# Kernel optimization log

Hardware: AMD Instinct MI355X
Metric: run time of the kernel (lower is better)

Reference implementation:

```python
import jax, jax.numpy as jnp
import numpy as np

K_MASK = -2.3819763e+38
NUM_HEADS = 16
NUM_KV_HEADS = 8
HEAD_DIM = 128
FEATURES = 2048
QUERY_SCALE = 0.08838834764831845  # head_dim ** -0.5
ROPE_BASE = 10000
SOFT_CAP = 50.0
WINDOW = 1024


def apply_rope(inputs, positions, base_frequency=ROPE_BASE):
    # inputs: [B, L, N, H], positions: [B, L]
    head_dim = inputs.shape[-1]
    fraction = 2.0 * jnp.arange(0, head_dim // 2, dtype=jnp.float32) / head_dim
    timescale = jnp.asarray(base_frequency, jnp.float32) ** fraction
    sinusoid = positions[..., None].astype(jnp.float32) / timescale[None, None, :]
    sinusoid = sinusoid[..., None, :]  # [B, L, 1, H/2]
    sin, cos = jnp.sin(sinusoid), jnp.cos(sinusoid)
    first, second = jnp.split(inputs, 2, axis=-1)
    out = jnp.concatenate([first * cos - second * sin,
                           second * cos + first * sin], axis=-1)
    return out.astype(inputs.dtype)


def setup_inputs() -> dict:
    key = jax.random.key(0)
    ks = jax.random.split(key, 4)
    B, T, D = 2, 2048, FEATURES
    x = jax.random.normal(ks[0], (B, T, D), dtype=jnp.float32)
    segment_pos = jnp.broadcast_to(jnp.arange(T, dtype=jnp.int32)[None, :], (B, T))
    # causal prefill mask [B, T, S] with S == T
    attn_mask = jnp.broadcast_to(
        jnp.tril(jnp.ones((T, T), dtype=bool))[None], (B, T, T))
    wq = jax.random.normal(ks[1], (NUM_HEADS, D, HEAD_DIM), dtype=jnp.float32) * 0.02
    wkv = jax.random.normal(ks[2], (2, NUM_KV_HEADS, D, HEAD_DIM), dtype=jnp.float32) * 0.02
    wo = jax.random.normal(ks[3], (NUM_HEADS, HEAD_DIM, D), dtype=jnp.float32) * 0.02
    return {"x": x, "segment_pos": segment_pos, "attn_mask": attn_mask,
            "wq": wq, "wkv": wkv, "wo": wo}


def reference(x, segment_pos, attn_mask, wq, wkv, wo):
    # Projections
    q = jnp.einsum('BTD,NDH->BTNH', x, wq)              # [B,T,N,H]
    kv = jnp.einsum('BSD,CKDH->CBSKH', x, wkv)          # [2,B,S,K,H]
    k, v = kv[0], kv[1]

    # RoPE + query scaling
    q = apply_rope(q, segment_pos) * QUERY_SCALE
    k = apply_rope(k, segment_pos)

    # GQA: fold query heads into (K groups, G heads per group)
    B, T, N, H = q.shape
    K, G = NUM_KV_HEADS, N // NUM_KV_HEADS
    qg = q.reshape(B, T, K, G, H)
    logits = jnp.einsum('BTKGH,BSKH->BTKGS', qg, k).reshape(B, T, N, -1)

    # Logit soft-capping
    logits = jnp.tanh(logits / SOFT_CAP) * SOFT_CAP

    # Sliding-window mask (prefill: end_index=0, cache_len = S)
    S = attn_mask.shape[-1]
    cache_positions = jnp.arange(S)[None, None, :]       # [1,1,S]
    sp = segment_pos[:, :, None]                         # [B,T,1]
    sliding = (cache_positions > sp - WINDOW) & (cache_positions < sp + WINDOW)
    mask = jnp.logical_and(attn_mask, sliding)

    padded = jnp.where(mask[:, :, None, :], logits, K_MASK)
    probs = jax.nn.softmax(padded, axis=-1).astype(k.dtype)

    pg = probs.reshape(B, T, K, G, S)
    encoded = jnp.einsum('BTKGS,BSKH->BTKGH', pg, v).reshape(B, T, N, H)
    return jnp.einsum('BTNH,NHD->BTD', encoded, wo)
```

## Files before the change

kernel.cpp:

```cpp
#include <hip/hip_runtime.h>

typedef __attribute__((ext_vector_type(8))) short short8;
typedef __attribute__((ext_vector_type(4))) float f32x4;
typedef __attribute__((ext_vector_type(4))) float f4;
typedef __attribute__((ext_vector_type(4))) unsigned short u16x4;

__device__ __forceinline__ unsigned short f2bf(float f) {
    union { float f; unsigned int u; } v; v.f = f;
    unsigned int r = v.u + 0x7fffu + ((v.u >> 16) & 1u);
    return (unsigned short)(r >> 16);
}
__device__ __forceinline__ float bf2f(unsigned short h) {
    union { unsigned int u; float f; } v; v.u = ((unsigned int)h) << 16;
    return v.f;
}
__device__ __forceinline__ void gload_lds16(const void* g, void* l) {
    __builtin_amdgcn_global_load_lds(
        (const __attribute__((address_space(1))) unsigned int*)g,
        (__attribute__((address_space(3))) unsigned int*)l, 16, 0, 0);
}


__global__ void conv_x(const float* __restrict__ x, unsigned short* __restrict__ xb) {
    int i = blockIdx.x * 256 + threadIdx.x;
    f4 v = ((const f4*)x)[i];
    u16x4 o;
    o[0] = f2bf(v[0]); o[1] = f2bf(v[1]); o[2] = f2bf(v[2]); o[3] = f2bf(v[3]);
    ((u16x4*)xb)[i] = o;
}

__global__ void conv_wqkvt(const float* __restrict__ wq, const float* __restrict__ wkv,
                           unsigned short* __restrict__ wt) {
    __shared__ float tile[64 * 65];
    const int d0 = blockIdx.x * 64, f0 = blockIdx.y * 64;
    const int head = f0 >> 7;
    const int h0 = f0 & 127;
    const float* src;
    if (head < 16) src = wq + (size_t)head * 2048 * 128;
    else           src = wkv + (size_t)(head - 16) * 2048 * 128;
    {
        int hh = threadIdx.x & 63, dq = threadIdx.x >> 6;
        #pragma unroll
        for (int r = 0; r < 16; ++r) {
            int dd = r * 4 + dq;
            tile[dd * 65 + hh] = src[(size_t)(d0 + dd) * 128 + h0 + hh];
        }
    }
    __syncthreads();
    {
        int dd = threadIdx.x & 63, fq = threadIdx.x >> 6;
        #pragma unroll
        for (int r = 0; r < 16; ++r) {
            int fl = r * 4 + fq;
            wt[(size_t)(f0 + fl) * 2048 + d0 + dd] = f2bf(tile[dd * 65 + fl]);
        }
    }
}

__global__ void conv_wot(const float* __restrict__ wo, unsigned short* __restrict__ wt) {
    __shared__ float tile[64 * 65];
    const int d0 = blockIdx.x * 64, r0 = blockIdx.y * 64;
    int cc = threadIdx.x & 63, rq = threadIdx.x >> 6;
    #pragma unroll
    for (int r = 0; r < 16; ++r) {
        int rr = r * 4 + rq;
        tile[rr * 65 + cc] = wo[(size_t)(r0 + rr) * 2048 + d0 + cc];
    }
    __syncthreads();
    #pragma unroll
    for (int r = 0; r < 16; ++r) {
        int rr = r * 4 + rq;
        wt[(size_t)(d0 + rr) * 2048 + r0 + cc] = f2bf(tile[cc * 65 + rr]);
    }
}


__global__ __launch_bounds__(512, 2)
void gemm8p(const unsigned short* __restrict__ A,
            const unsigned short* __restrict__ Bt,
            unsigned short* __restrict__ C, int M, int N, int K) {
    __shared__ __align__(16) unsigned short LDS[65536];
    const int tid = threadIdx.x, lane = tid & 63, w = tid >> 6;
    const int wr = w >> 2, wc = w & 3;
    const int l15 = lane & 15, l4 = lane >> 4;
    int nwg = gridDim.x * gridDim.y;
    int wg = blockIdx.y * gridDim.x + blockIdx.x;
    int swz = (wg & 7) * (nwg >> 3) + (wg >> 3);
    int bx = swz % gridDim.x, by = swz / gridDim.x;
    const int brow = by * 256, bcol = bx * 256;
    const int wg_a = w & 3;
    const int wg_b = wr;
    const int rA = wg_a * 8 + (lane >> 3);
    const int rB = wg_b * 8 + (lane >> 3);
    const int cgS = ((lane & 7) ^ (lane >> 3)) * 8;
    const unsigned short* aP = A + (size_t)(brow + wr * 128 + rA) * K + cgS;
    const unsigned short* bP = Bt + (size_t)(bcol + wc * 64 + rB) * K + cgS;
    const int ldsA0 = wr * 8192 + (wg_a * 64 + lane) * 8;
    const int ldsB0 = wc * 4096 + (wg_b * 64 + lane) * 8;
    const int aRd = (wr * 128 + l15) * 64;
    const int bRd = (wc * 64 + l15) * 64;
    const int c0 = ((0 + l4) ^ (l15 & 7)) * 8;
    const int c1 = ((4 + l4) ^ (l15 & 7)) * 8;
    f32x4 acc[8][4] = {};
    const int nt = K >> 6;
    gload_lds16(aP,                  &LDS[ldsA0]);
    gload_lds16(bP,                  &LDS[16384 + ldsB0]);
    gload_lds16(aP + (size_t)32 * K, &LDS[ldsA0 + 2048]);
    gload_lds16(bP + (size_t)16 * K, &LDS[16384 + ldsB0 + 1024]);
    gload_lds16(bP + (size_t)32 * K, &LDS[16384 + ldsB0 + 2048]);
    gload_lds16(bP + (size_t)48 * K, &LDS[16384 + ldsB0 + 3072]);
    gload_lds16(aP + (size_t)64 * K, &LDS[ldsA0 + 4096]);
    gload_lds16(aP + (size_t)96 * K, &LDS[ldsA0 + 6144]);
    asm volatile("s_waitcnt vmcnt(4)" ::: "memory");
    __builtin_amdgcn_s_barrier();
    __builtin_amdgcn_sched_barrier(0);

    short8 af[4][2], bl[2][2], bh[2][2];
    for (int t = 0; t < nt; ++t) {
        const int bufA = (t & 1) << 15, bufB = bufA + 16384;
        const bool pf = (t + 1) < nt;
        const int sA = ((t + 1) & 1) << 15, sB = sA + 16384;
        const unsigned short* ap = aP + (t + 1) * 64;
        const unsigned short* bp = bP + (t + 1) * 64;
        #pragma unroll
        for (int m = 0; m < 4; ++m) {
            af[m][0] = *(const short8*)&LDS[bufA + aRd + m * 1024 + c0];
            af[m][1] = *(const short8*)&LDS[bufA + aRd + m * 1024 + c1];
        }
        #pragma unroll
        for (int n = 0; n < 2; ++n) {
            bl[n][0] = *(const short8*)&LDS[bufB + bRd + n * 1024 + c0];
            bl[n][1] = *(const short8*)&LDS[bufB + bRd + n * 1024 + c1];
        }
        if (pf) { gload_lds16(ap, &LDS[sA + ldsA0]);
                  gload_lds16(bp, &LDS[sB + ldsB0]); }
        __builtin_amdgcn_s_barrier();
        __builtin_amdgcn_sched_barrier(0);
        __builtin_amdgcn_s_setprio(1);
        #pragma unroll
        for (int m = 0; m < 4; ++m)
            #pragma unroll
            for (int n = 0; n < 2; ++n) {
                acc[m][n] = __builtin_amdgcn_mfma_f32_16x16x32_bf16(af[m][0], bl[n][0], acc[m][n], 0, 0, 0);
                acc[m][n] = __builtin_amdgcn_mfma_f32_16x16x32_bf16(af[m][1], bl[n][1], acc[m][n], 0, 0, 0);
            }
        __builtin_amdgcn_s_setprio(0);
        asm volatile("s_waitcnt vmcnt(4)" ::: "memory");
        __builtin_amdgcn_s_barrier();
        __builtin_amdgcn_sched_barrier(0);
        #pragma unroll
        for (int n = 0; n < 2; ++n) {
            bh[n][0] = *(const short8*)&LDS[bufB + bRd + (n + 2) * 1024 + c0];
            bh[n][1] = *(const short8*)&LDS[bufB + bRd + (n + 2) * 1024 + c1];
        }
        if (pf) { gload_lds16(ap + (size_t)32 * K, &LDS[sA + ldsA0 + 2048]);
                  gload_lds16(bp + (size_t)16 * K, &LDS[sB + ldsB0 + 1024]); }
        __builtin_amdgcn_s_barrier();
        __builtin_amdgcn_sched_barrier(0);
        __builtin_amdgcn_s_setprio(1);
        #pragma unroll
        for (int m = 0; m < 4; ++m)
            #pragma unroll
            for (int n = 0; n < 2; ++n) {
                acc[m][n + 2] = __builtin_amdgcn_mfma_f32_16x16x32_bf16(af[m][0], bh[n][0], acc[m][n + 2], 0, 0, 0);
                acc[m][n + 2] = __builtin_amdgcn_mfma_f32_16x16x32_bf16(af[m][1], bh[n][1], acc[m][n + 2], 0, 0, 0);
            }
        __builtin_amdgcn_s_setprio(0);
        asm volatile("s_waitcnt vmcnt(4)" ::: "memory");
        __builtin_amdgcn_s_barrier();
        __builtin_amdgcn_sched_barrier(0);
        #pragma unroll
        for (int m = 0; m < 4; ++m) {
            af[m][0] = *(const short8*)&LDS[bufA + aRd + (m + 4) * 1024 + c0];
            af[m][1] = *(const short8*)&LDS[bufA + aRd + (m + 4) * 1024 + c1];
        }
        if (pf) { gload_lds16(bp + (size_t)32 * K, &LDS[sB + ldsB0 + 2048]);
                  gload_lds16(bp + (size_t)48 * K, &LDS[sB + ldsB0 + 3072]); }
        __builtin_amdgcn_s_barrier();
        __builtin_amdgcn_sched_barrier(0);
        __builtin_amdgcn_s_setprio(1);
        #pragma unroll
        for (int m = 0; m < 4; ++m)
            #pragma unroll
            for (int n = 0; n < 2; ++n) {
                acc[m + 4][n] = __builtin_amdgcn_mfma_f32_16x16x32_bf16(af[m][0], bl[n][0], acc[m + 4][n], 0, 0, 0);
                acc[m + 4][n] = __builtin_amdgcn_mfma_f32_16x16x32_bf16(af[m][1], bl[n][1], acc[m + 4][n], 0, 0, 0);
            }
        __builtin_amdgcn_s_setprio(0);
        __builtin_amdgcn_s_barrier();
        __builtin_amdgcn_sched_barrier(0);
        if (pf) { gload_lds16(ap + (size_t)64 * K, &LDS[sA + ldsA0 + 4096]);
                  gload_lds16(ap + (size_t)96 * K, &LDS[sA + ldsA0 + 6144]); }
        __builtin_amdgcn_s_barrier();
        __builtin_amdgcn_sched_barrier(0);
        __builtin_amdgcn_s_setprio(1);
        #pragma unroll
        for (int m = 0; m < 4; ++m)
            #pragma unroll
            for (int n = 0; n < 2; ++n) {
                acc[m + 4][n + 2] = __builtin_amdgcn_mfma_f32_16x16x32_bf16(af[m][0], bh[n][0], acc[m + 4][n + 2], 0, 0, 0);
                acc[m + 4][n + 2] = __builtin_amdgcn_mfma_f32_16x16x32_bf16(af[m][1], bh[n][1], acc[m + 4][n + 2], 0, 0, 0);
            }
        __builtin_amdgcn_s_setprio(0);
        asm volatile("s_waitcnt vmcnt(4)" ::: "memory");
        __builtin_amdgcn_s_barrier();
        __builtin_amdgcn_sched_barrier(0);
    }
    #pragma unroll
    for (int m = 0; m < 8; ++m)
        #pragma unroll
        for (int n = 0; n < 4; ++n)
            #pragma unroll
            for (int j = 0; j < 4; ++j) {
                int row = brow + wr * 128 + m * 16 + l4 * 4 + j;
                int col = bcol + wc * 64 + n * 16 + l15;
                C[(size_t)row * N + col] = f2bf(acc[m][n][j]);
            }
}


__global__ __launch_bounds__(512, 1)
void gemm8p_n128(const unsigned short* __restrict__ A,
                 const unsigned short* __restrict__ Bt,
                 float* __restrict__ C, int M, int N, int K) {
    __shared__ __align__(16) unsigned short LDS[49152];
    const int tid = threadIdx.x, lane = tid & 63, w = tid >> 6;
    const int wr = w >> 2, wc = w & 3;
    const int l15 = lane & 15, l4 = lane >> 4;
    int nwg = gridDim.x * gridDim.y;
    int wg = blockIdx.y * gridDim.x + blockIdx.x;
    int swz = (wg & 7) * (nwg >> 3) + (wg >> 3);
    int bx = swz % gridDim.x, by = swz / gridDim.x;
    const int brow = by * 256, bcol = bx * 128;
    const int wg_a = w & 3;
    const int wg_b = wr;
    const int rA = wg_a * 8 + (lane >> 3);
    const int rB = wg_b * 8 + (lane >> 3);
    const int cgS = ((lane & 7) ^ (lane >> 3)) * 8;
    const unsigned short* aP = A + (size_t)(brow + wr * 128 + rA) * K + cgS;
    const unsigned short* bP = Bt + (size_t)(bcol + wc * 32 + rB) * K + cgS;
    const int ldsA0 = wr * 8192 + (wg_a * 64 + lane) * 8;
    const int ldsB0 = wc * 2048 + (wg_b * 64 + lane) * 8;
    const int aRd = (wr * 128 + l15) * 64;
    const int bRd = (wc * 32 + l15) * 64;
    const int c0 = ((0 + l4) ^ (l15 & 7)) * 8;
    const int c1 = ((4 + l4) ^ (l15 & 7)) * 8;
    f32x4 acc[8][2] = {};
    const int nt = K >> 6;
    gload_lds16(aP,                  &LDS[ldsA0]);
    gload_lds16(bP,                  &LDS[16384 + ldsB0]);
    gload_lds16(aP + (size_t)32 * K, &LDS[ldsA0 + 2048]);
    gload_lds16(bP + (size_t)16 * K, &LDS[16384 + ldsB0 + 1024]);
    gload_lds16(aP + (size_t)64 * K, &LDS[ldsA0 + 4096]);
    gload_lds16(aP + (size_t)96 * K, &LDS[ldsA0 + 6144]);
    asm volatile("s_waitcnt vmcnt(3)" ::: "memory");
    __builtin_amdgcn_s_barrier();
    __builtin_amdgcn_sched_barrier(0);
    short8 afl[4][2], afh[4][2], bl0[2], bl1[2];
    for (int t = 0; t < nt; ++t) {
        const int bufA = (t & 1) * 24576, bufB = bufA + 16384;
        const bool pf = (t + 1) < nt;
        const int sA = ((t + 1) & 1) * 24576, sB = sA + 16384;
        const unsigned short* ap = aP + (t + 1) * 64;
        const unsigned short* bp = bP + (t + 1) * 64;
        #pragma unroll
        for (int m = 0; m < 4; ++m) {
            afl[m][0] = *(const short8*)&LDS[bufA + aRd + m * 1024 + c0];
            afl[m][1] = *(const short8*)&LDS[bufA + aRd + m * 1024 + c1];
        }
        bl0[0] = *(const short8*)&LDS[bufB + bRd + c0];
        bl0[1] = *(const short8*)&LDS[bufB + bRd + c1];
        if (pf) { gload_lds16(ap, &LDS[sA + ldsA0]);
                  gload_lds16(bp, &LDS[sB + ldsB0]); }
        __builtin_amdgcn_s_barrier();
        __builtin_amdgcn_sched_barrier(0);
        __builtin_amdgcn_s_setprio(1);
        #pragma unroll
        for (int m = 0; m < 4; ++m) {
            acc[m][0] = __builtin_amdgcn_mfma_f32_16x16x32_bf16(afl[m][0], bl0[0], acc[m][0], 0, 0, 0);
            acc[m][0] = __builtin_amdgcn_mfma_f32_16x16x32_bf16(afl[m][1], bl0[1], acc[m][0], 0, 0, 0);
        }
        __builtin_amdgcn_s_setprio(0);
        asm volatile("s_waitcnt vmcnt(4)" ::: "memory");
        __builtin_amdgcn_s_barrier();
        __builtin_amdgcn_sched_barrier(0);
        bl1[0] = *(const short8*)&LDS[bufB + bRd + 1024 + c0];
        bl1[1] = *(const short8*)&LDS[bufB + bRd + 1024 + c1];
        if (pf) { gload_lds16(ap + (size_t)32 * K, &LDS[sA + ldsA0 + 2048]);
                  gload_lds16(bp + (size_t)16 * K, &LDS[sB + ldsB0 + 1024]); }
        __builtin_amdgcn_s_barrier();
        __builtin_amdgcn_sched_barrier(0);
        __builtin_amdgcn_s_setprio(1);
        #pragma unroll
        for (int m = 0; m < 4; ++m) {
            acc[m][1] = __builtin_amdgcn_mfma_f32_16x16x32_bf16(afl[m][0], bl1[0], acc[m][1], 0, 0, 0);
            acc[m][1] = __builtin_amdgcn_mfma_f32_16x16x32_bf16(afl[m][1], bl1[1], acc[m][1], 0, 0, 0);
        }
        __builtin_amdgcn_s_setprio(0);
        asm volatile("s_waitcnt vmcnt(4)" ::: "memory");
        __builtin_amdgcn_s_barrier();
        __builtin_amdgcn_sched_barrier(0);
        #pragma unroll
        for (int m = 0; m < 4; ++m) {
            afh[m][0] = *(const short8*)&LDS[bufA + aRd + (m + 4) * 1024 + c0];
            afh[m][1] = *(const short8*)&LDS[bufA + aRd + (m + 4) * 1024 + c1];
        }
        if (pf) gload_lds16(ap + (size_t)64 * K, &LDS[sA + ldsA0 + 4096]);
        __builtin_amdgcn_s_barrier();
        __builtin_amdgcn_sched_barrier(0);
        __builtin_amdgcn_s_setprio(1);
        #pragma unroll
        for (int m = 0; m < 4; ++m) {
            acc[m + 4][0] = __builtin_amdgcn_mfma_f32_16x16x32_bf16(afh[m][0], bl0[0], acc[m + 4][0], 0, 0, 0);
            acc[m + 4][0] = __builtin_amdgcn_mfma_f32_16x16x32_bf16(afh[m][1], bl0[1], acc[m + 4][0], 0, 0, 0);
        }
        __builtin_amdgcn_s_setprio(0);
        __builtin_amdgcn_s_barrier();
        __builtin_amdgcn_sched_barrier(0);
        if (pf) gload_lds16(ap + (size_t)96 * K, &LDS[sA + ldsA0 + 6144]);
        __builtin_amdgcn_s_barrier();
        __builtin_amdgcn_sched_barrier(0);
        __builtin_amdgcn_s_setprio(1);
        #pragma unroll
        for (int m = 0; m < 4; ++m) {
            acc[m + 4][1] = __builtin_amdgcn_mfma_f32_16x16x32_bf16(afh[m][0], bl1[0], acc[m + 4][1], 0, 0, 0);
            acc[m + 4][1] = __builtin_amdgcn_mfma_f32_16x16x32_bf16(afh[m][1], bl1[1], acc[m + 4][1], 0, 0, 0);
        }
        __builtin_amdgcn_s_setprio(0);
        asm volatile("s_waitcnt vmcnt(3)" ::: "memory");
        __builtin_amdgcn_s_barrier();
        __builtin_amdgcn_sched_barrier(0);
    }
    #pragma unroll
    for (int m = 0; m < 8; ++m)
        #pragma unroll
        for (int n = 0; n < 2; ++n)
            #pragma unroll
            for (int j = 0; j < 4; ++j) {
                int row = brow + wr * 128 + m * 16 + l4 * 4 + j;
                int col = bcol + wc * 32 + n * 16 + l15;
                C[(size_t)row * N + col] = acc[m][n][j];
            }
}

__global__ void rope_reshape(const unsigned short* __restrict__ qkv,
                             const int* __restrict__ segpos,
                             unsigned short* __restrict__ q_r,
                             unsigned short* __restrict__ k_r) {
    const int bt = blockIdx.x;
    const int hd = blockIdx.y * 2 + (threadIdx.x >> 7);
    const int b = bt >> 11, t = bt & 2047;
    const int h = threadIdx.x & 127;
    const unsigned short* in = (hd < 16)
        ? qkv + (size_t)bt * 4096 + hd * 128
        : qkv + (size_t)bt * 4096 + 2048 + (hd - 16) * 128;
    int pos = segpos[bt];
    int i = h & 63;
    float inv_ts = __expf((float)i * (-9.210340371976184f / 64.f));
    float ang = (float)pos * inv_ts;
    float s = __sinf(ang), c = __cosf(ang);
    float x1 = bf2f(in[i]);
    float x2 = bf2f(in[i + 64]);
    float o = (h < 64) ? (x1 * c - x2 * s) : (x2 * c + x1 * s);
    if (hd < 16) {
        o *= 0.08838834764831845f;
        q_r[((size_t)((b * 16 + hd) * 2048 + t)) * 128 + h] = f2bf(o);
    } else {
        int kh = hd - 16;
        k_r[((size_t)((b * 8 + kh) * 2048 + t)) * 128 + h] = f2bf(o);
    }
}

__global__ void v_transpose(const unsigned short* __restrict__ qkv,
                            unsigned short* __restrict__ v_t) {
    __shared__ unsigned short tile[64][72];
    const int tt0 = blockIdx.x * 64;
    const int kh = blockIdx.y >> 1, hb = (blockIdx.y & 1) * 64;
    const int b = blockIdx.z;
    int c = threadIdx.x & 63, rq = threadIdx.x >> 6;
    #pragma unroll
    for (int r = 0; r < 16; ++r) {
        int tt = r * 4 + rq;
        tile[tt][c] = qkv[(size_t)(b * 2048 + tt0 + tt) * 4096 + 3072 + kh * 128 + hb + c];
    }
    __syncthreads();
    #pragma unroll
    for (int r = 0; r < 16; ++r) {
        int hr = r * 4 + rq;
        v_t[((size_t)(b * 8 + kh) * 128 + hb + hr) * 2048 + tt0 + c] = tile[c][hr];
    }
}


__device__ __forceinline__ void stage_kv(const unsigned short* kbase, const unsigned short* vbase,
                                         unsigned short* Ksb, unsigned short* Vtb,
                                         int st, int tid) {
    #pragma unroll
    for (int r = 0; r < 2; ++r) {
        int e = (r * 512 + tid) * 8;
        int krow = e >> 7, kcol = e & 127;
        gload_lds16(kbase + (size_t)(st * 64 + krow) * 128 + (kcol ^ ((krow & 7) << 3)), Ksb + e);
        int vrow = e >> 6, vcol = e & 63;
        gload_lds16(vbase + (size_t)vrow * 2048 + st * 64 + (vcol ^ ((vrow & 7) << 3)), Vtb + e);
    }
}

__global__ __launch_bounds__(512, 4)
void attn_kernel(const unsigned short* __restrict__ q_r,
                 const unsigned short* __restrict__ k_r,
                 const unsigned short* __restrict__ v_t,
                 unsigned short* __restrict__ enc) {
    __shared__ __align__(16) unsigned short Ks[2][64 * 128];
    __shared__ __align__(16) unsigned short Vt[2][128 * 64];
    __shared__ __align__(16) unsigned short Pl[8][16 * 64];
    const int tid = threadIdx.x, lane = tid & 63, wave = tid >> 6;
    const int l15 = lane & 15, l4 = lane >> 4;
    const int flat = blockIdx.x;
    const int xcd = flat & 7, g = flat >> 3;
    const int pair = xcd * 2 + (g >> 5);
    const int qb = 31 - (g & 31);
    const int kh = pair >> 1, b = pair & 1;
    const int n = kh * 2 + (wave >> 2);
    const int wq = wave & 3;
    short8 qf[4];
    {
        const unsigned short* qp =
            q_r + ((size_t)((b * 16 + n) * 2048 + qb * 64 + wq * 16 + l15)) * 128 + l4 * 8;
        #pragma unroll
        for (int kk = 0; kk < 4; ++kk) qf[kk] = *(const short8*)(qp + kk * 32);
    }
    f32x4 Of[8] = {};
    float lrow[4] = {};
    int t_lo = qb * 64 - 1023; if (t_lo < 0) t_lo = 0;
    const int st0 = t_lo >> 6;
    const unsigned short* kbase = k_r + (size_t)(b * 8 + kh) * 2048 * 128;
    const unsigned short* vbase = v_t + (size_t)(b * 8 + kh) * 128 * 2048;

    stage_kv(kbase, vbase, Ks[0], Vt[0], st0, tid);
    __syncthreads();
    int cur = 0;
    for (int st = st0; st <= qb; ++st) {
        if (st < qb)
            stage_kv(kbase, vbase, Ks[cur ^ 1], Vt[cur ^ 1], st + 1, tid);
        f32x4 sf[4] = {};
        #pragma unroll
        for (int nc = 0; nc < 4; ++nc) {
            int row = nc * 16 + l15;
            int sw = (l15 & 7) << 3;
            #pragma unroll
            for (int kk = 0; kk < 4; ++kk) {
                short8 bfr = *(const short8*)&Ks[cur][row * 128 + ((kk * 32 + l4 * 8) ^ sw)];
                sf[nc] = __builtin_amdgcn_mfma_f32_16x16x32_bf16(qf[kk], bfr, sf[nc], 0, 0, 0);
            }
        }
        const int mode = (st == qb) ? 1 : ((qb >= 16 && st == st0) ? 2 : 0);
        #pragma unroll
        for (int j = 0; j < 4; ++j) {
            int trow = qb * 64 + wq * 16 + l4 * 4 + j;
            int prow = l4 * 4 + j;
            int psw = (prow & 7) << 3;
            #pragma unroll
            for (int nc = 0; nc < 4; ++nc) {
                float ex = __expf(sf[nc][j] * 0.04f);
                float p = __expf(-100.f * __builtin_amdgcn_rcpf(ex + 1.f));
                if (mode) {
                    int s = st * 64 + nc * 16 + l15;
                    bool ok = (mode == 1) ? (s <= trow) : (s >= trow - 1023);
                    p = ok ? p : 0.f;
                }
                lrow[j] += p;
                Pl[wave][prow * 64 + ((nc * 16 + l15) ^ psw)] = f2bf(p);
            }
        }
        {
            int asw = (l15 & 7) << 3;
            #pragma unroll
            for (int ks = 0; ks < 2; ++ks) {
                short8 af = *(const short8*)&Pl[wave][l15 * 64 + ((ks * 32 + l4 * 8) ^ asw)];
                #pragma unroll
                for (int hc = 0; hc < 8; ++hc) {
                    int vrow = hc * 16 + l15;
                    short8 bfr = *(const short8*)&Vt[cur][vrow * 64 + ((ks * 32 + l4 * 8) ^ asw)];
                    Of[hc] = __builtin_amdgcn_mfma_f32_16x16x32_bf16(af, bfr, Of[hc], 0, 0, 0);
                }
            }
        }
        __syncthreads();
        cur ^= 1;
    }
    float inv[4];
    #pragma unroll
    for (int j = 0; j < 4; ++j) {
        float l = lrow[j];
        l += __shfl_xor(l, 1); l += __shfl_xor(l, 2);
        l += __shfl_xor(l, 4); l += __shfl_xor(l, 8);
        inv[j] = 1.f / l;
    }
    #pragma unroll
    for (int hc = 0; hc < 8; ++hc)
        #pragma unroll
        for (int j = 0; j < 4; ++j) {
            size_t row = (size_t)(b * 2048 + qb * 64 + wq * 16 + l4 * 4 + j);
            enc[row * 2048 + n * 128 + hc * 16 + l15] = f2bf(Of[hc][j] * inv[j]);
        }
}


extern "C" void kernel_launch(void* const* d_in, const int* in_sizes, int n_in,
                              void* d_out, int out_size, void* d_ws, size_t ws_size,
                              hipStream_t stream) {
    const float* x   = (const float*)d_in[0];
    const int* segp  = (const int*)d_in[1];
    const float* wq  = (const float*)d_in[3];
    const float* wkv = (const float*)d_in[4];
    const float* wo  = (const float*)d_in[5];
    float* out = (float*)d_out;
    char* ws = (char*)d_ws;
    if (ws_size < ((size_t)96 << 20)) return;

    unsigned short* xb    = (unsigned short*)(ws);
    unsigned short* wqkvt = (unsigned short*)(ws + ((size_t)16 << 20));
    unsigned short* qkv   = (unsigned short*)(ws + ((size_t)32 << 20));
    unsigned short* q_r   = (unsigned short*)(ws + ((size_t)64 << 20));
    unsigned short* k_r   = (unsigned short*)(ws + ((size_t)80 << 20));
    unsigned short* v_t   = (unsigned short*)(ws + ((size_t)88 << 20));
    unsigned short* wo_t  = (unsigned short*)(ws);
    unsigned short* enc   = (unsigned short*)(ws + ((size_t)32 << 20));

    conv_x<<<8192, 256, 0, stream>>>(x, xb);
    conv_wqkvt<<<dim3(32, 64), 256, 0, stream>>>(wq, wkv, wqkvt);
    gemm8p<<<dim3(16, 16), 512, 0, stream>>>(xb, wqkvt, qkv, 4096, 4096, 2048);
    rope_reshape<<<dim3(4096, 12), 256, 0, stream>>>(qkv, segp, q_r, k_r);
    v_transpose<<<dim3(32, 16, 2), 256, 0, stream>>>(qkv, v_t);
    conv_wot<<<dim3(32, 32), 256, 0, stream>>>(wo, wo_t);
    attn_kernel<<<512, 512, 0, stream>>>(q_r, k_r, v_t, enc);
    gemm8p_n128<<<dim3(16, 16), 512, 0, stream>>>(enc, wo_t, out, 4096, 2048, 2048);
}
```

Measured before the change: 208.3 us.

## Split-K output projection through generic gemm8p and reorder MFMA loops

Removes the dedicated 256x128-tile output-projection GEMM. The output projection now reuses the 256x256-tile gemm8p with a two-way split-K, writing bf16 partial results that a new addparts kernel sums into the fp32 output. gemm8p is generalized with leading-dimension, tile-count and slice arguments. Its MFMA loops and the attention QK loop are reordered so that k-chunk iterations are outermost, which spaces out dependent accumulations on the same register. The split-K adds an extra partial write/read pass and rounds partial sums to bf16, which costs some output precision.

New measurement: 216.7 us. 4.1% more time.

```diff
diff --git a/kernel.cpp b/kernel.cpp
--- a/kernel.cpp
+++ b/kernel.cpp
@@ -78,7 +78,8 @@
 __global__ __launch_bounds__(512, 2)
 void gemm8p(const unsigned short* __restrict__ A,
             const unsigned short* __restrict__ Bt,
-            unsigned short* __restrict__ C, int M, int N, int K) {
+            unsigned short* __restrict__ C,
+            int ldk, int ldc, int nt, int ksplit, size_t cstride) {
     __shared__ __align__(16) unsigned short LDS[65536];
     const int tid = threadIdx.x, lane = tid & 63, w = tid >> 6;
     const int wr = w >> 2, wc = w & 3;
@@ -87,14 +88,18 @@
     int wg = blockIdx.y * gridDim.x + blockIdx.x;
     int swz = (wg & 7) * (nwg >> 3) + (wg >> 3);
     int bx = swz % gridDim.x, by = swz / gridDim.x;
+    int slice = 0;
+    if (ksplit) { slice = by & 1; by >>= 1; }
+    unsigned short* Cs = C + (size_t)slice * cstride;
     const int brow = by * 256, bcol = bx * 256;
+    const size_t koff = (size_t)slice * nt * 64;
     const int wg_a = w & 3;
     const int wg_b = wr;
     const int rA = wg_a * 8 + (lane >> 3);
     const int rB = wg_b * 8 + (lane >> 3);
     const int cgS = ((lane & 7) ^ (lane >> 3)) * 8;
-    const unsigned short* aP = A + (size_t)(brow + wr * 128 + rA) * K + cgS;
-    const unsigned short* bP = Bt + (size_t)(bcol + wc * 64 + rB) * K + cgS;
+    const unsigned short* aP = A + (size_t)(brow + wr * 128 + rA) * ldk + koff + cgS;
+    const unsigned short* bP = Bt + (size_t)(bcol + wc * 64 + rB) * ldk + koff + cgS;
     const int ldsA0 = wr * 8192 + (wg_a * 64 + lane) * 8;
     const int ldsB0 = wc * 4096 + (wg_b * 64 + lane) * 8;
     const int aRd = (wr * 128 + l15) * 64;
@@ -102,15 +107,14 @@
     const int c0 = ((0 + l4) ^ (l15 & 7)) * 8;
     const int c1 = ((4 + l4) ^ (l15 & 7)) * 8;
     f32x4 acc[8][4] = {};
-    const int nt = K >> 6;
-    gload_lds16(aP,                  &LDS[ldsA0]);
-    gload_lds16(bP,                  &LDS[16384 + ldsB0]);
-    gload_lds16(aP + (size_t)32 * K, &LDS[ldsA0 + 2048]);
-    gload_lds16(bP + (size_t)16 * K, &LDS[16384 + ldsB0 + 1024]);
-    gload_lds16(bP + (size_t)32 * K, &LDS[16384 + ldsB0 + 2048]);
-    gload_lds16(bP + (size_t)48 * K, &LDS[16384 + ldsB0 + 3072]);
-    gload_lds16(aP + (size_t)64 * K, &LDS[ldsA0 + 4096]);
-    gload_lds16(aP + (size_t)96 * K, &LDS[ldsA0 + 6144]);
+    gload_lds16(aP,                    &LDS[ldsA0]);
+    gload_lds16(bP,                    &LDS[16384 + ldsB0]);
+    gload_lds16(aP + (size_t)32 * ldk, &LDS[ldsA0 + 2048]);
+    gload_lds16(bP + (size_t)16 * ldk, &LDS[16384 + ldsB0 + 1024]);
+    gload_lds16(bP + (size_t)32 * ldk, &LDS[16384 + ldsB0 + 2048]);
+    gload_lds16(bP + (size_t)48 * ldk, &LDS[16384 + ldsB0 + 3072]);
+    gload_lds16(aP + (size_t)64 * ldk, &LDS[ldsA0 + 4096]);
+    gload_lds16(aP + (size_t)96 * ldk, &LDS[ldsA0 + 6144]);
     asm volatile("s_waitcnt vmcnt(4)" ::: "memory");
     __builtin_amdgcn_s_barrier();
     __builtin_amdgcn_sched_barrier(0);
@@ -138,12 +142,12 @@
         __builtin_amdgcn_sched_barrier(0);
         __builtin_amdgcn_s_setprio(1);
         #pragma unroll
-        for (int m = 0; m < 4; ++m)
-            #pragma unroll
-            for (int n = 0; n < 2; ++n) {
-                acc[m][n] = __builtin_amdgcn_mfma_f32_16x16x32_bf16(af[m][0], bl[n][0], acc[m][n], 0, 0, 0);
-                acc[m][n] = __builtin_amdgcn_mfma_f32_16x16x32_bf16(af[m][1], bl[n][1], acc[m][n], 0, 0, 0);
-            }
+        for (int kk = 0; kk < 2; ++kk)
+            #pragma unroll
+            for (int m = 0; m < 4; ++m)
+                #pragma unroll
+                for (int n = 0; n < 2; ++n)
+                    acc[m][n] = __builtin_amdgcn_mfma_f32_16x16x32_bf16(af[m][kk], bl[n][kk], acc[m][n], 0, 0, 0);
         __builtin_amdgcn_s_setprio(0);
         asm volatile("s_waitcnt vmcnt(4)" ::: "memory");
         __builtin_amdgcn_s_barrier();
@@ -153,18 +157,18 @@
             bh[n][0] = *(const short8*)&LDS[bufB + bRd + (n + 2) * 1024 + c0];
             bh[n][1] = *(const short8*)&LDS[bufB + bRd + (n + 2) * 1024 + c1];
         }
-        if (pf) { gload_lds16(ap + (size_t)32 * K, &LDS[sA + ldsA0 + 2048]);
-                  gload_lds16(bp + (size_t)16 * K, &LDS[sB + ldsB0 + 1024]); }
+        if (pf) { gload_lds16(ap + (size_t)32 * ldk, &LDS[sA + ldsA0 + 2048]);
+                  gload_lds16(bp + (size_t)16 * ldk, &LDS[sB + ldsB0 + 1024]); }
         __builtin_amdgcn_s_barrier();
         __builtin_amdgcn_sched_barrier(0);
         __builtin_amdgcn_s_setprio(1);
         #pragma unroll
-        for (int m = 0; m < 4; ++m)
-            #pragma unroll
-            for (int n = 0; n < 2; ++n) {
-                acc[m][n + 2] = __builtin_amdgcn_mfma_f32_16x16x32_bf16(af[m][0], bh[n][0], acc[m][n + 2], 0, 0, 0);
-                acc[m][n + 2] = __builtin_amdgcn_mfma_f32_16x16x32_bf16(af[m][1], bh[n][1], acc[m][n + 2], 0, 0, 0);
-            }
+        for (int kk = 0; kk < 2; ++kk)
+            #pragma unroll
+            for (int m = 0; m < 4; ++m)
+                #pragma unroll
+                for (int n = 0; n < 2; ++n)
+                    acc[m][n + 2] = __builtin_amdgcn_mfma_f32_16x16x32_bf16(af[m][kk], bh[n][kk], acc[m][n + 2], 0, 0, 0);
         __builtin_amdgcn_s_setprio(0);
         asm volatile("s_waitcnt vmcnt(4)" ::: "memory");
         __builtin_amdgcn_s_barrier();
@@ -174,33 +178,33 @@
             af[m][0] = *(const short8*)&LDS[bufA + aRd + (m + 4) * 1024 + c0];
             af[m][1] = *(const short8*)&LDS[bufA + aRd + (m + 4) * 1024 + c1];
         }
-        if (pf) { gload_lds16(bp + (size_t)32 * K, &LDS[sB + ldsB0 + 2048]);
-                  gload_lds16(bp + (size_t)48 * K, &LDS[sB + ldsB0 + 3072]); }
+        if (pf) { gload_lds16(bp + (size_t)32 * ldk, &LDS[sB + ldsB0 + 2048]);
+                  gload_lds16(bp + (size_t)48 * ldk, &LDS[sB + ldsB0 + 3072]); }
         __builtin_amdgcn_s_barrier();
         __builtin_amdgcn_sched_barrier(0);
         __builtin_amdgcn_s_setprio(1);
         #pragma unroll
-        for (int m = 0; m < 4; ++m)
-            #pragma unroll
-            for (int n = 0; n < 2; ++n) {
-                acc[m + 4][n] = __builtin_amdgcn_mfma_f32_16x16x32_bf16(af[m][0], bl[n][0], acc[m + 4][n], 0, 0, 0);
-                acc[m + 4][n] = __builtin_amdgcn_mfma_f32_16x16x32_bf16(af[m][1], bl[n][1], acc[m + 4][n], 0, 0, 0);
-            }
+        for (int kk = 0; kk < 2; ++kk)
+            #pragma unroll
+            for (int m = 0; m < 4; ++m)
+                #pragma unroll
+                for (int n = 0; n < 2; ++n)
+                    acc[m + 4][n] = __builtin_amdgcn_mfma_f32_16x16x32_bf16(af[m][kk], bl[n][kk], acc[m + 4][n], 0, 0, 0);
         __builtin_amdgcn_s_setprio(0);
         __builtin_amdgcn_s_barrier();
         __builtin_amdgcn_sched_barrier(0);
-        if (pf) { gload_lds16(ap + (size_t)64 * K, &LDS[sA + ldsA0 + 4096]);
-                  gload_lds16(ap + (size_t)96 * K, &LDS[sA + ldsA0 + 6144]); }
+        if (pf) { gload_lds16(ap + (size_t)64 * ldk, &LDS[sA + ldsA0 + 4096]);
+                  gload_lds16(ap + (size_t)96 * ldk, &LDS[sA + ldsA0 + 6144]); }
         __builtin_amdgcn_s_barrier();
         __builtin_amdgcn_sched_barrier(0);
         __builtin_amdgcn_s_setprio(1);
         #pragma unroll
-        for (int m = 0; m < 4; ++m)
-            #pragma unroll
-            for (int n = 0; n < 2; ++n) {
-                acc[m + 4][n + 2] = __builtin_amdgcn_mfma_f32_16x16x32_bf16(af[m][0], bh[n][0], acc[m + 4][n + 2], 0, 0, 0);
-                acc[m + 4][n + 2] = __builtin_amdgcn_mfma_f32_16x16x32_bf16(af[m][1], bh[n][1], acc[m + 4][n + 2], 0, 0, 0);
-            }
+        for (int kk = 0; kk < 2; ++kk)
+            #pragma unroll
+            for (int m = 0; m < 4; ++m)
+                #pragma unroll
+                for (int n = 0; n < 2; ++n)
+                    acc[m + 4][n + 2] = __builtin_amdgcn_mfma_f32_16x16x32_bf16(af[m][kk], bh[n][kk], acc[m + 4][n + 2], 0, 0, 0);
         __builtin_amdgcn_s_setprio(0);
         asm volatile("s_waitcnt vmcnt(4)" ::: "memory");
         __builtin_amdgcn_s_barrier();
@@ -214,133 +218,25 @@
             for (int j = 0; j < 4; ++j) {
                 int row = brow + wr * 128 + m * 16 + l4 * 4 + j;
                 int col = bcol + wc * 64 + n * 16 + l15;
-                C[(size_t)row * N + col] = f2bf(acc[m][n][j]);
+                Cs[(size_t)row * ldc + col] = f2bf(acc[m][n][j]);
             }
 }
 
-
-__global__ __launch_bounds__(512, 1)
-void gemm8p_n128(const unsigned short* __restrict__ A,
-                 const unsigned short* __restrict__ Bt,
-                 float* __restrict__ C, int M, int N, int K) {
-    __shared__ __align__(16) unsigned short LDS[49152];
-    const int tid = threadIdx.x, lane = tid & 63, w = tid >> 6;
-    const int wr = w >> 2, wc = w & 3;
-    const int l15 = lane & 15, l4 = lane >> 4;
-    int nwg = gridDim.x * gridDim.y;
-    int wg = blockIdx.y * gridDim.x + blockIdx.x;
-    int swz = (wg & 7) * (nwg >> 3) + (wg >> 3);
-    int bx = swz % gridDim.x, by = swz / gridDim.x;
-    const int brow = by * 256, bcol = bx * 128;
-    const int wg_a = w & 3;
-    const int wg_b = wr;
-    const int rA = wg_a * 8 + (lane >> 3);
-    const int rB = wg_b * 8 + (lane >> 3);
-    const int cgS = ((lane & 7) ^ (lane >> 3)) * 8;
-    const unsigned short* aP = A + (size_t)(brow + wr * 128 + rA) * K + cgS;
-    const unsigned short* bP = Bt + (size_t)(bcol + wc * 32 + rB) * K + cgS;
-    const int ldsA0 = wr * 8192 + (wg_a * 64 + lane) * 8;
-    const int ldsB0 = wc * 2048 + (wg_b * 64 + lane) * 8;
-    const int aRd = (wr * 128 + l15) * 64;
-    const int bRd = (wc * 32 + l15) * 64;
-    const int c0 = ((0 + l4) ^ (l15 & 7)) * 8;
-    const int c1 = ((4 + l4) ^ (l15 & 7)) * 8;
-    f32x4 acc[8][2] = {};
-    const int nt = K >> 6;
-    gload_lds16(aP,                  &LDS[ldsA0]);
-    gload_lds16(bP,                  &LDS[16384 + ldsB0]);
-    gload_lds16(aP + (size_t)32 * K, &LDS[ldsA0 + 2048]);
-    gload_lds16(bP + (size_t)16 * K, &LDS[16384 + ldsB0 + 1024]);
-    gload_lds16(aP + (size_t)64 * K, &LDS[ldsA0 + 4096]);
-    gload_lds16(aP + (size_t)96 * K, &LDS[ldsA0 + 6144]);
-    asm volatile("s_waitcnt vmcnt(3)" ::: "memory");
-    __builtin_amdgcn_s_barrier();
-    __builtin_amdgcn_sched_barrier(0);
-    short8 afl[4][2], afh[4][2], bl0[2], bl1[2];
-    for (int t = 0; t < nt; ++t) {
-        const int bufA = (t & 1) * 24576, bufB = bufA + 16384;
-        const bool pf = (t + 1) < nt;
-        const int sA = ((t + 1) & 1) * 24576, sB = sA + 16384;
-        const unsigned short* ap = aP + (t + 1) * 64;
-        const unsigned short* bp = bP + (t + 1) * 64;
-        #pragma unroll
-        for (int m = 0; m < 4; ++m) {
-            afl[m][0] = *(const short8*)&LDS[bufA + aRd + m * 1024 + c0];
-            afl[m][1] = *(const short8*)&LDS[bufA + aRd + m * 1024 + c1];
-        }
-        bl0[0] = *(const short8*)&LDS[bufB + bRd + c0];
-        bl0[1] = *(const short8*)&LDS[bufB + bRd + c1];
-        if (pf) { gload_lds16(ap, &LDS[sA + ldsA0]);
-                  gload_lds16(bp, &LDS[sB + ldsB0]); }
-        __builtin_amdgcn_s_barrier();
-        __builtin_amdgcn_sched_barrier(0);
-        __builtin_amdgcn_s_setprio(1);
-        #pragma unroll
-        for (int m = 0; m < 4; ++m) {
-            acc[m][0] = __builtin_amdgcn_mfma_f32_16x16x32_bf16(afl[m][0], bl0[0], acc[m][0], 0, 0, 0);
-            acc[m][0] = __builtin_amdgcn_mfma_f32_16x16x32_bf16(afl[m][1], bl0[1], acc[m][0], 0, 0, 0);
-        }
-        __builtin_amdgcn_s_setprio(0);
-        asm volatile("s_waitcnt vmcnt(4)" ::: "memory");
-        __builtin_amdgcn_s_barrier();
-        __builtin_amdgcn_sched_barrier(0);
-        bl1[0] = *(const short8*)&LDS[bufB + bRd + 1024 + c0];
-        bl1[1] = *(const short8*)&LDS[bufB + bRd + 1024 + c1];
-        if (pf) { gload_lds16(ap + (size_t)32 * K, &LDS[sA + ldsA0 + 2048]);
-                  gload_lds16(bp + (size_t)16 * K, &LDS[sB + ldsB0 + 1024]); }
-        __builtin_amdgcn_s_barrier();
-        __builtin_amdgcn_sched_barrier(0);
-        __builtin_amdgcn_s_setprio(1);
-        #pragma unroll
-        for (int m = 0; m < 4; ++m) {
-            acc[m][1] = __builtin_amdgcn_mfma_f32_16x16x32_bf16(afl[m][0], bl1[0], acc[m][1], 0, 0, 0);
-            acc[m][1] = __builtin_amdgcn_mfma_f32_16x16x32_bf16(afl[m][1], bl1[1], acc[m][1], 0, 0, 0);
-        }
-        __builtin_amdgcn_s_setprio(0);
-        asm volatile("s_waitcnt vmcnt(4)" ::: "memory");
-        __builtin_amdgcn_s_barrier();
-        __builtin_amdgcn_sched_barrier(0);
-        #pragma unroll
-        for (int m = 0; m < 4; ++m) {
-            afh[m][0] = *(const short8*)&LDS[bufA + aRd + (m + 4) * 1024 + c0];
-            afh[m][1] = *(const short8*)&LDS[bufA + aRd + (m + 4) * 1024 + c1];
-        }
-        if (pf) gload_lds16(ap + (size_t)64 * K, &LDS[sA + ldsA0 + 4096]);
-        __builtin_amdgcn_s_barrier();
-        __builtin_amdgcn_sched_barrier(0);
-        __builtin_amdgcn_s_setprio(1);
-        #pragma unroll
-        for (int m = 0; m < 4; ++m) {
-            acc[m + 4][0] = __builtin_amdgcn_mfma_f32_16x16x32_bf16(afh[m][0], bl0[0], acc[m + 4][0], 0, 0, 0);
-            acc[m + 4][0] = __builtin_amdgcn_mfma_f32_16x16x32_bf16(afh[m][1], bl0[1], acc[m + 4][0], 0, 0, 0);
-        }
-        __builtin_amdgcn_s_setprio(0);
-        __builtin_amdgcn_s_barrier();
-        __builtin_amdgcn_sched_barrier(0);
-        if (pf) gload_lds16(ap + (size_t)96 * K, &LDS[sA + ldsA0 + 6144]);
-        __builtin_amdgcn_s_barrier();
-        __builtin_amdgcn_sched_barrier(0);
-        __builtin_amdgcn_s_setprio(1);
-        #pragma unroll
-        for (int m = 0; m < 4; ++m) {
-            acc[m + 4][1] = __builtin_amdgcn_mfma_f32_16x16x32_bf16(afh[m][0], bl1[0], acc[m + 4][1], 0, 0, 0);
-            acc[m + 4][1] = __builtin_amdgcn_mfma_f32_16x16x32_bf16(afh[m][1], bl1[1], acc[m + 4][1], 0, 0, 0);
-        }
-        __builtin_amdgcn_s_setprio(0);
-        asm volatile("s_waitcnt vmcnt(3)" ::: "memory");
-        __builtin_amdgcn_s_barrier();
-        __builtin_amdgcn_sched_barrier(0);
-    }
-    #pragma unroll
-    for (int m = 0; m < 8; ++m)
-        #pragma unroll
-        for (int n = 0; n < 2; ++n)
-            #pragma unroll
-            for (int j = 0; j < 4; ++j) {
-                int row = brow + wr * 128 + m * 16 + l4 * 4 + j;
-                int col = bcol + wc * 32 + n * 16 + l15;
-                C[(size_t)row * N + col] = acc[m][n][j];
-            }
+__global__ void addparts(const unsigned short* __restrict__ p0,
+                         const unsigned short* __restrict__ p1,
+                         float* __restrict__ out) {
+    int i = blockIdx.x * 256 + threadIdx.x;
+    short8 a = ((const short8*)p0)[i];
+    short8 b = ((const short8*)p1)[i];
+    f4 lo, hi;
+    #pragma unroll
+    for (int j = 0; j < 4; ++j)
+        lo[j] = bf2f((unsigned short)a[j]) + bf2f((unsigned short)b[j]);
+    #pragma unroll
+    for (int j = 0; j < 4; ++j)
+        hi[j] = bf2f((unsigned short)a[j + 4]) + bf2f((unsigned short)b[j + 4]);
+    ((f4*)out)[2 * i] = lo;
+    ((f4*)out)[2 * i + 1] = hi;
 }
 
 __global__ void rope_reshape(const unsigned short* __restrict__ qkv,
@@ -443,15 +339,15 @@
         if (st < qb)
             stage_kv(kbase, vbase, Ks[cur ^ 1], Vt[cur ^ 1], st + 1, tid);
         f32x4 sf[4] = {};
-        #pragma unroll
-        for (int nc = 0; nc < 4; ++nc) {
-            int row = nc * 16 + l15;
+        {
             int sw = (l15 & 7) << 3;
             #pragma unroll
-            for (int kk = 0; kk < 4; ++kk) {
-                short8 bfr = *(const short8*)&Ks[cur][row * 128 + ((kk * 32 + l4 * 8) ^ sw)];
-                sf[nc] = __builtin_amdgcn_mfma_f32_16x16x32_bf16(qf[kk], bfr, sf[nc], 0, 0, 0);
-            }
+            for (int kk = 0; kk < 4; ++kk)
+                #pragma unroll
+                for (int nc = 0; nc < 4; ++nc) {
+                    short8 bfr = *(const short8*)&Ks[cur][(nc * 16 + l15) * 128 + ((kk * 32 + l4 * 8) ^ sw)];
+                    sf[nc] = __builtin_amdgcn_mfma_f32_16x16x32_bf16(qf[kk], bfr, sf[nc], 0, 0, 0);
+                }
         }
         const int mode = (st == qb) ? 1 : ((qb >= 16 && st == st0) ? 2 : 0);
         #pragma unroll
@@ -524,15 +420,17 @@
     unsigned short* q_r   = (unsigned short*)(ws + ((size_t)64 << 20));
     unsigned short* k_r   = (unsigned short*)(ws + ((size_t)80 << 20));
     unsigned short* v_t   = (unsigned short*)(ws + ((size_t)88 << 20));
-    unsigned short* wo_t  = (unsigned short*)(ws);
+    unsigned short* wo_t  = (unsigned short*)(ws + ((size_t)16 << 20));
     unsigned short* enc   = (unsigned short*)(ws + ((size_t)32 << 20));
+    unsigned short* part  = (unsigned short*)(ws + ((size_t)64 << 20));
 
     conv_x<<<8192, 256, 0, stream>>>(x, xb);
     conv_wqkvt<<<dim3(32, 64), 256, 0, stream>>>(wq, wkv, wqkvt);
-    gemm8p<<<dim3(16, 16), 512, 0, stream>>>(xb, wqkvt, qkv, 4096, 4096, 2048);
+    gemm8p<<<dim3(16, 16), 512, 0, stream>>>(xb, wqkvt, qkv, 2048, 4096, 32, 0, 0);
     rope_reshape<<<dim3(4096, 12), 256, 0, stream>>>(qkv, segp, q_r, k_r);
     v_transpose<<<dim3(32, 16, 2), 256, 0, stream>>>(qkv, v_t);
     conv_wot<<<dim3(32, 32), 256, 0, stream>>>(wo, wo_t);
     attn_kernel<<<512, 512, 0, stream>>>(q_r, k_r, v_t, enc);
-    gemm8p_n128<<<dim3(16, 16), 512, 0, stream>>>(enc, wo_t, out, 4096, 2048, 2048);
-}
+    gemm8p<<<dim3(8, 32), 512, 0, stream>>>(enc, wo_t, part, 2048, 2048, 16, 1, (size_t)4096 * 2048);
+    addparts<<<4096, 256, 0, stream>>>(part, part + (size_t)4096 * 2048, out);
+}
```
